# Performance work log

Hardware: AMD Instinct MI355X
Metric: run time of the kernel (lower is better)

Reference implementation:

```python
import jax, jax.numpy as jnp
import numpy as np

H = 128  # hidden size

def lstm_layer(x, Wih, Whh, bih, bhh):
    """One PyTorch-semantics LSTM layer. x: (B,T,F). Gate order: i,f,g,o."""
    B = x.shape[0]
    # Precompute input contributions for all timesteps: (B,T,4H)
    xg = jnp.einsum('btf,gf->btg', x, Wih) + bih + bhh
    def step(carry, xt):
        h, c = carry
        g = xt + h @ Whh.T                      # (B,4H)
        i, f, gg, o = jnp.split(g, 4, axis=-1)
        i = jax.nn.sigmoid(i)
        f = jax.nn.sigmoid(f)
        gg = jnp.tanh(gg)
        o = jax.nn.sigmoid(o)
        c = f * c + i * gg
        h = o * jnp.tanh(c)
        return (h, c), h
    h0 = jnp.zeros((B, H), x.dtype)
    (hT, cT), hs = jax.lax.scan(step, (h0, h0), jnp.swapaxes(xg, 0, 1))
    return jnp.swapaxes(hs, 0, 1), hT  # (B,T,H), (B,H)


def setup_inputs() -> dict:
    key = jax.random.key(0)
    ks = jax.random.split(key, 20)
    B, T = 256, 2048
    s = 1.0 / np.sqrt(H)  # PyTorch default init scale
    inp = {
        'x': jax.random.normal(ks[0], (B, T, 1), jnp.float32),
        'Wih0': jax.random.uniform(ks[1], (4 * H, 1), jnp.float32, -s, s),
        'Whh0': jax.random.uniform(ks[2], (4 * H, H), jnp.float32, -s, s),
        'bih0': jax.random.uniform(ks[3], (4 * H,), jnp.float32, -s, s),
        'bhh0': jax.random.uniform(ks[4], (4 * H,), jnp.float32, -s, s),
        'Wih1': jax.random.uniform(ks[5], (4 * H, H), jnp.float32, -s, s),
        'Whh1': jax.random.uniform(ks[6], (4 * H, H), jnp.float32, -s, s),
        'bih1': jax.random.uniform(ks[7], (4 * H,), jnp.float32, -s, s),
        'bhh1': jax.random.uniform(ks[8], (4 * H,), jnp.float32, -s, s),
        'Wih2': jax.random.uniform(ks[9], (4 * H, H), jnp.float32, -s, s),
        'Whh2': jax.random.uniform(ks[10], (4 * H, H), jnp.float32, -s, s),
        'bih2': jax.random.uniform(ks[11], (4 * H,), jnp.float32, -s, s),
        'bhh2': jax.random.uniform(ks[12], (4 * H,), jnp.float32, -s, s),
        'fc1_w': jax.random.uniform(ks[13], (64, H), jnp.float32, -s, s),
        'fc1_b': jax.random.uniform(ks[14], (64,), jnp.float32, -s, s),
        'fc2_w': jax.random.uniform(ks[15], (5, 64), jnp.float32, -1.0 / 8, 1.0 / 8),
        'fc2_b': jax.random.uniform(ks[16], (5,), jnp.float32, -1.0 / 8, 1.0 / 8),
    }
    return inp


def reference(x, Wih0, Whh0, bih0, bhh0, Wih1, Whh1, bih1, bhh1,
              Wih2, Whh2, bih2, bhh2, fc1_w, fc1_b, fc2_w, fc2_b):
    # 3-layer LSTM (eval mode: inter-layer dropout is identity)
    h1, _ = lstm_layer(x, Wih0, Whh0, bih0, bhh0)
    h2, _ = lstm_layer(h1, Wih1, Whh1, bih1, bhh1)
    _, hT = lstm_layer(h2, Wih2, Whh2, bih2, bhh2)  # hn[-1]: (B,H)
    z = jax.nn.relu(hT @ fc1_w.T + fc1_b)
    return z @ fc2_w.T + fc2_b  # (B, num_classes)
```

## Files before the change

### kernel.cpp

```cpp
#include <hip/hip_runtime.h>

#define HDIM 128
#define TDIM 2048
#define BDIM 256
#define CHUNK 16
#define NT 512
#define XGP 20

typedef _Float16 half8_t __attribute__((ext_vector_type(8)));
typedef float f32x4 __attribute__((ext_vector_type(4)));

__device__ __forceinline__ f32x4 mfma16(half8_t a, half8_t b, f32x4 c) {
    return __builtin_amdgcn_mfma_f32_16x16x32_f16(a, b, c, 0, 0, 0);
}

__device__ __forceinline__ void fast_barrier() {
    asm volatile("s_waitcnt lgkmcnt(0)\n\ts_barrier" ::: "memory");
}

__device__ __forceinline__ float sigm_f(float x) { return 1.0f / (1.0f + __expf(-x)); }
__device__ __forceinline__ float tanh_f(float x) { return 1.0f - 2.0f / (1.0f + __expf(2.0f * x)); }

__global__ __launch_bounds__(256)
void convert_w(const float* __restrict__ Whh0, const float* __restrict__ Wih1,
               const float* __restrict__ Whh1, const float* __restrict__ Wih2,
               const float* __restrict__ Whh2, _Float16* __restrict__ dst) {
    int i = blockIdx.x * 256 + threadIdx.x;
    int seg = i >> 16, off = i & 65535;
    const float* s = (seg == 0) ? Whh0 : (seg == 1) ? Wih1 : (seg == 2) ? Whh1
                   : (seg == 3) ? Wih2 : Whh2;
    dst[i] = (_Float16)s[off];
}

__global__ __launch_bounds__(NT, 2)
void lstm3_kernel(const float* __restrict__ x,   const float* __restrict__ Wih0,
                  const float* __restrict__ bih0, const float* __restrict__ bhh0,
                  const float* __restrict__ bih1, const float* __restrict__ bhh1,
                  const float* __restrict__ bih2, const float* __restrict__ bhh2,
                  const float* __restrict__ fc1w, const float* __restrict__ fc1b,
                  const float* __restrict__ fc2w, const float* __restrict__ fc2b,
                  float* __restrict__ out,
                  _Float16* __restrict__ gbuf, const _Float16* __restrict__ wbuf)
{
    __shared__ __align__(16) _Float16 hwin_s[CHUNK][HDIM];
    __shared__ __align__(16) _Float16 xin_s[2][CHUNK][HDIM];
    __shared__ __align__(16) float xg_s[2][512 * XGP];
    __shared__ __align__(16) float z_s[64];

    const int tid = threadIdx.x;
    const int ln = tid & 63;
    const int wv = tid >> 6;
    const int n16 = ln & 15;
    const int kb = (ln >> 4) * 8;
    const int un = wv * 16 + n16;
    const int b = blockIdx.x;

    {
        float bsum[4], w0[4];
        half8_t bhh[4][4];
#pragma unroll
        for (int tau = 0; tau < 4; ++tau) {
            const int g = tau * HDIM + un;
            bsum[tau] = bih0[g] + bhh0[g];
            w0[tau] = Wih0[g];
#pragma unroll
            for (int kk = 0; kk < 4; ++kk)
                bhh[tau][kk] = *(const half8_t*)(wbuf + (size_t)g * HDIM + kk * 32 + kb);
        }
        if (tid < HDIM) hwin_s[CHUNK - 1][tid] = (_Float16)0.f;
        float c = 0.f;
        float4 xp[4];
        {
            const float4* xq = (const float4*)(x + (size_t)b * TDIM);
#pragma unroll
            for (int i = 0; i < 4; ++i) xp[i] = xq[i];
        }

#pragma unroll 1
        for (int t0 = 0; t0 < TDIM; t0 += CHUNK) {
            float xv[CHUNK];
#pragma unroll
            for (int i = 0; i < 4; ++i) {
                xv[4 * i] = xp[i].x; xv[4 * i + 1] = xp[i].y;
                xv[4 * i + 2] = xp[i].z; xv[4 * i + 3] = xp[i].w;
            }
            int tn = (t0 + CHUNK < TDIM) ? (t0 + CHUNK) : t0;
            const float4* xq = (const float4*)(x + (size_t)b * TDIM + tn);
#pragma unroll
            for (int i = 0; i < 4; ++i) xp[i] = xq[i];

#pragma unroll
            for (int tt = 0; tt < CHUNK; ++tt) {
                fast_barrier();
                const int t = t0 + tt, row = (t + CHUNK - 1) & 15;
                half8_t A0 = *(const half8_t*)&hwin_s[row][kb];
                half8_t A1 = *(const half8_t*)&hwin_s[row][32 + kb];
                half8_t A2 = *(const half8_t*)&hwin_s[row][64 + kb];
                half8_t A3 = *(const half8_t*)&hwin_s[row][96 + kb];
                float g4[4];
#pragma unroll
                for (int tau = 0; tau < 4; ++tau) {
                    f32x4 Cz = {0.f, 0.f, 0.f, 0.f};
                    Cz = mfma16(A0, bhh[tau][0], Cz);
                    Cz = mfma16(A1, bhh[tau][1], Cz);
                    Cz = mfma16(A2, bhh[tau][2], Cz);
                    Cz = mfma16(A3, bhh[tau][3], Cz);
                    g4[tau] = Cz[0];
                }
                float ig = sigm_f(g4[0] + xv[tt] * w0[0] + bsum[0]);
                float fg = sigm_f(g4[1] + xv[tt] * w0[1] + bsum[1]);
                float gg = tanh_f(g4[2] + xv[tt] * w0[2] + bsum[2]);
                float og = sigm_f(g4[3] + xv[tt] * w0[3] + bsum[3]);
                c = fg * c + ig * gg;
                if (kb == 0) hwin_s[t & 15][un] = (_Float16)(og * tanh_f(c));
            }
            fast_barrier();
            int2 v = ((const int2*)&hwin_s[0][0])[tid];
            ((int2*)(gbuf + ((size_t)b * TDIM + t0) * HDIM))[tid] = v;
        }
    }

#pragma unroll 1
    for (int layer = 1; layer < 3; ++layer) {
        const _Float16* whh_p = wbuf + (size_t)((layer == 1) ? 2 : 4) * 65536;
        const _Float16* wih_p = wbuf + (size_t)((layer == 1) ? 1 : 3) * 65536;
        const float* bih = (layer == 1) ? bih1 : bih2;
        const float* bhh = (layer == 1) ? bhh1 : bhh2;

        float bsum[4];
        half8_t bhhf[4][4], bihf[4][4];
#pragma unroll
        for (int tau = 0; tau < 4; ++tau) {
            const int g = tau * HDIM + un;
            bsum[tau] = bih[g] + bhh[g];
#pragma unroll
            for (int kk = 0; kk < 4; ++kk)
                bhhf[tau][kk] = *(const half8_t*)(whh_p + (size_t)g * HDIM + kk * 32 + kb);
            const int gp = (wv * 4 + tau) * 16 + n16;
#pragma unroll
            for (int kk = 0; kk < 4; ++kk)
                bihf[tau][kk] = *(const half8_t*)(wih_p + (size_t)gp * HDIM + kk * 32 + kb);
        }

        __syncthreads();
        if (tid < HDIM) hwin_s[CHUNK - 1][tid] = (_Float16)0.f;
        float c = 0.f;

        int2 stage = ((const int2*)(gbuf + (size_t)b * TDIM * HDIM))[tid];
        ((int2*)&xin_s[0][0][0])[tid] = stage;
        __syncthreads();
        {
            half8_t A0 = *(const half8_t*)&xin_s[0][n16][kb];
            half8_t A1 = *(const half8_t*)&xin_s[0][n16][32 + kb];
            half8_t A2 = *(const half8_t*)&xin_s[0][n16][64 + kb];
            half8_t A3 = *(const half8_t*)&xin_s[0][n16][96 + kb];
#pragma unroll
            for (int tau = 0; tau < 4; ++tau) {
                f32x4 a = {0.f, 0.f, 0.f, 0.f};
                a = mfma16(A0, bihf[tau][0], a);
                a = mfma16(A1, bihf[tau][1], a);
                a = mfma16(A2, bihf[tau][2], a);
                a = mfma16(A3, bihf[tau][3], a);
                const int g = (wv * 4 + tau) * 16 + n16;
                *(f32x4*)&xg_s[0][g * XGP + (kb >> 1)] = a;
            }
        }
        stage = ((const int2*)(gbuf + ((size_t)b * TDIM + CHUNK) * HDIM))[tid];

        f32x4 pacc[4];
#pragma unroll 1
        for (int t0 = 0; t0 < TDIM; t0 += CHUNK) {
            const int ci = t0 >> 4, rbuf = ci & 1, cb = rbuf ^ 1;
            ((int2*)&xin_s[cb][0][0])[tid] = stage;
            int tn = (t0 + 2 * CHUNK < TDIM) ? (t0 + 2 * CHUNK) : t0;
            stage = ((const int2*)(gbuf + ((size_t)b * TDIM + tn) * HDIM))[tid];

            float2 xgv[4];
#pragma unroll
            for (int tt = 0; tt < CHUNK; ++tt) {
                fast_barrier();
                const int t = t0 + tt, row = (t + CHUNK - 1) & 15;
                half8_t A0 = *(const half8_t*)&hwin_s[row][kb];
                half8_t A1 = *(const half8_t*)&hwin_s[row][32 + kb];
                half8_t A2 = *(const half8_t*)&hwin_s[row][64 + kb];
                half8_t A3 = *(const half8_t*)&hwin_s[row][96 + kb];

                if (tt == 0) {
                    half8_t X0 = *(const half8_t*)&xin_s[cb][n16][kb];
                    half8_t X1 = *(const half8_t*)&xin_s[cb][n16][32 + kb];
                    half8_t X2 = *(const half8_t*)&xin_s[cb][n16][64 + kb];
                    half8_t X3 = *(const half8_t*)&xin_s[cb][n16][96 + kb];
#pragma unroll
                    for (int tau = 0; tau < 4; ++tau) {
                        f32x4 a = {0.f, 0.f, 0.f, 0.f};
                        a = mfma16(X0, bihf[tau][0], a);
                        a = mfma16(X1, bihf[tau][1], a);
                        a = mfma16(X2, bihf[tau][2], a);
                        a = mfma16(X3, bihf[tau][3], a);
                        pacc[tau] = a;
                    }
                }
                if ((tt & 1) == 0) {
#pragma unroll
                    for (int q = 0; q < 4; ++q)
                        xgv[q] = *(const float2*)&xg_s[rbuf][(q * HDIM + un) * XGP + tt];
                }

                float g4[4];
#pragma unroll
                for (int tau = 0; tau < 4; ++tau) {
                    f32x4 Cz = {0.f, 0.f, 0.f, 0.f};
                    Cz = mfma16(A0, bhhf[tau][0], Cz);
                    Cz = mfma16(A1, bhhf[tau][1], Cz);
                    Cz = mfma16(A2, bhhf[tau][2], Cz);
                    Cz = mfma16(A3, bhhf[tau][3], Cz);
                    g4[tau] = Cz[0];
                }

                float x0 = (tt & 1) ? xgv[0].y : xgv[0].x;
                float x1 = (tt & 1) ? xgv[1].y : xgv[1].x;
                float x2 = (tt & 1) ? xgv[2].y : xgv[2].x;
                float x3 = (tt & 1) ? xgv[3].y : xgv[3].x;
                float ig = sigm_f(g4[0] + x0 + bsum[0]);
                float fg = sigm_f(g4[1] + x1 + bsum[1]);
                float gg = tanh_f(g4[2] + x2 + bsum[2]);
                float og = sigm_f(g4[3] + x3 + bsum[3]);
                c = fg * c + ig * gg;
                if (kb == 0) hwin_s[t & 15][un] = (_Float16)(og * tanh_f(c));

                if (tt == CHUNK - 1) {
#pragma unroll
                    for (int tau = 0; tau < 4; ++tau) {
                        const int g = (wv * 4 + tau) * 16 + n16;
                        *(f32x4*)&xg_s[cb][g * XGP + (kb >> 1)] = pacc[tau];
                    }
                }
            }
            if (layer == 1) {
                fast_barrier();
                int2 v = ((const int2*)&hwin_s[0][0])[tid];
                ((int2*)(gbuf + ((size_t)b * TDIM + t0) * HDIM))[tid] = v;
            }
        }
    }

    __syncthreads();
    if (tid < 64) {
        const float* w = fc1w + tid * HDIM;
        float s = fc1b[tid];
#pragma unroll
        for (int k = 0; k < HDIM; ++k) s += w[k] * (float)hwin_s[CHUNK - 1][k];
        z_s[tid] = fmaxf(s, 0.0f);
    }
    __syncthreads();
    if (tid < 5) {
        const float* w = fc2w + tid * 64;
        float s = fc2b[tid];
#pragma unroll
        for (int k = 0; k < 64; ++k) s += w[k] * z_s[k];
        out[b * 5 + tid] = s;
    }
}

extern "C" void kernel_launch(void* const* d_in, const int* in_sizes, int n_in,
                              void* d_out, int out_size, void* d_ws, size_t ws_size,
                              hipStream_t stream) {
    (void)in_sizes; (void)n_in; (void)out_size; (void)ws_size;
    const float* x    = (const float*)d_in[0];
    const float* Wih0 = (const float*)d_in[1];
    const float* Whh0 = (const float*)d_in[2];
    const float* bih0 = (const float*)d_in[3];
    const float* bhh0 = (const float*)d_in[4];
    const float* Wih1 = (const float*)d_in[5];
    const float* Whh1 = (const float*)d_in[6];
    const float* bih1 = (const float*)d_in[7];
    const float* bhh1 = (const float*)d_in[8];
    const float* Wih2 = (const float*)d_in[9];
    const float* Whh2 = (const float*)d_in[10];
    const float* bih2 = (const float*)d_in[11];
    const float* bhh2 = (const float*)d_in[12];
    const float* fc1w = (const float*)d_in[13];
    const float* fc1b = (const float*)d_in[14];
    const float* fc2w = (const float*)d_in[15];
    const float* fc2b = (const float*)d_in[16];
    float* out = (float*)d_out;

    _Float16* gbuf = (_Float16*)d_ws;
    _Float16* wbuf = gbuf + (size_t)67108864;

    hipLaunchKernelGGL(convert_w, dim3(1280), dim3(256), 0, stream,
                       Whh0, Wih1, Whh1, Wih2, Whh2, wbuf);
    hipLaunchKernelGGL(lstm3_kernel, dim3(BDIM), dim3(NT), 0, stream,
                       x, Wih0, bih0, bhh0, bih1, bhh1, bih2, bhh2,
                       fc1w, fc1b, fc2w, fc2b, out, gbuf, wbuf);
}
```

Measured before the change: 3.658 ms.

## Halve block to 256 threads, two hidden units per lane, Whh pinned in AGPRs

The block shrinks from 8 to 4 waves, so each lane now handles two hidden units. The recurrent Whh fragments are pinned in accumulator registers and fed to MFMA through inline asm. The input-projection weights are no longer held in registers; they are reloaded from global memory once per chunk. The goal is to cut per-step barrier cost and wave count on the serial recurrence, and the three layers are merged into one loop. In exchange each wave does twice the MFMA and activation work per step, adds hand-inserted s_nop hazard padding, and adds extra global loads for Wih.

```diff
diff --git a/kernel.cpp b/kernel.cpp
--- a/kernel.cpp
+++ b/kernel.cpp
@@ -3,8 +3,8 @@
 #define HDIM 128
 #define TDIM 2048
 #define BDIM 256
+#define NT 256
 #define CHUNK 16
-#define NT 512
 #define XGP 20
 
 typedef _Float16 half8_t __attribute__((ext_vector_type(8)));
@@ -13,6 +13,10 @@
 __device__ __forceinline__ f32x4 mfma16(half8_t a, half8_t b, f32x4 c) {
     return __builtin_amdgcn_mfma_f32_16x16x32_f16(a, b, c, 0, 0, 0);
 }
+__device__ __forceinline__ void mfma_agpr(f32x4 &d, half8_t a, half8_t b) {
+    asm("v_mfma_f32_16x16x32_f16 %0, %1, %2, %0" : "+v"(d) : "v"(a), "a"(b));
+}
+__device__ __forceinline__ void pin_agpr(half8_t &v) { asm("" : "+a"(v)); }
 
 __device__ __forceinline__ void fast_barrier() {
     asm volatile("s_waitcnt lgkmcnt(0)\n\ts_barrier" ::: "memory");
@@ -32,7 +36,7 @@
     dst[i] = (_Float16)s[off];
 }
 
-__global__ __launch_bounds__(NT, 2)
+__global__ __launch_bounds__(NT, 1)
 void lstm3_kernel(const float* __restrict__ x,   const float* __restrict__ Wih0,
                   const float* __restrict__ bih0, const float* __restrict__ bhh0,
                   const float* __restrict__ bih1, const float* __restrict__ bhh1,
@@ -47,48 +51,96 @@
     __shared__ __align__(16) float xg_s[2][512 * XGP];
     __shared__ __align__(16) float z_s[64];
 
-    const int tid = threadIdx.x;
-    const int ln = tid & 63;
-    const int wv = tid >> 6;
-    const int n16 = ln & 15;
-    const int kb = (ln >> 4) * 8;
-    const int un = wv * 16 + n16;
+    const int tid = threadIdx.x, ln = tid & 63, wv = tid >> 6;
+    const int n16 = ln & 15, qd = ln >> 4, kb = qd * 8;
+    const int un0 = wv * 32 + n16, un1 = un0 + 16;
     const int b = blockIdx.x;
 
-    {
-        float bsum[4], w0[4];
-        half8_t bhh[4][4];
-#pragma unroll
-        for (int tau = 0; tau < 4; ++tau) {
-            const int g = tau * HDIM + un;
-            bsum[tau] = bih0[g] + bhh0[g];
-            w0[tau] = Wih0[g];
-#pragma unroll
-            for (int kk = 0; kk < 4; ++kk)
-                bhh[tau][kk] = *(const half8_t*)(wbuf + (size_t)g * HDIM + kk * 32 + kb);
+    const _Float16* whhL[3] = {wbuf, wbuf + 2 * 65536, wbuf + 4 * 65536};
+    const _Float16* wihL[3] = {nullptr, wbuf + 1 * 65536, wbuf + 3 * 65536};
+    const float* bihL[3] = {bih0, bih1, bih2};
+    const float* bhhL[3] = {bhh0, bhh1, bhh2};
+
+    half8_t whh[2][4][4];
+
+#pragma unroll 1
+    for (int layer = 0; layer < 3; ++layer) {
+        float bsum[2][4], w0[2][4];
+#pragma unroll
+        for (int ug = 0; ug < 2; ++ug) {
+            const int un = (ug == 0) ? un0 : un1;
+#pragma unroll
+            for (int q = 0; q < 4; ++q) {
+                const int row = q * HDIM + un;
+                bsum[ug][q] = bihL[layer][row] + bhhL[layer][row];
+                w0[ug][q] = (layer == 0) ? Wih0[row] : 0.f;
+#pragma unroll
+                for (int kk = 0; kk < 4; ++kk) {
+                    whh[ug][q][kk] =
+                        *(const half8_t*)(whhL[layer] + (size_t)row * HDIM + kk * 32 + kb);
+                    pin_agpr(whh[ug][q][kk]);
+                }
+            }
         }
+
+        __syncthreads();
         if (tid < HDIM) hwin_s[CHUNK - 1][tid] = (_Float16)0.f;
-        float c = 0.f;
+        float c0 = 0.f, c1 = 0.f;
+
         float4 xp[4];
-        {
+        int4 stage = {0, 0, 0, 0};
+        if (layer == 0) {
             const float4* xq = (const float4*)(x + (size_t)b * TDIM);
 #pragma unroll
             for (int i = 0; i < 4; ++i) xp[i] = xq[i];
+            __syncthreads();
+        } else {
+            stage = ((const int4*)(gbuf + (size_t)b * TDIM * HDIM))[tid];
+            ((int4*)&xin_s[0][0][0])[tid] = stage;
+            __syncthreads();
+            half8_t X0 = *(const half8_t*)&xin_s[0][n16][kb];
+            half8_t X1 = *(const half8_t*)&xin_s[0][n16][32 + kb];
+            half8_t X2 = *(const half8_t*)&xin_s[0][n16][64 + kb];
+            half8_t X3 = *(const half8_t*)&xin_s[0][n16][96 + kb];
+#pragma unroll 1
+            for (int j = 0; j < 8; ++j) {
+                const int gp = (8 * wv + j) * 16 + n16;
+                const _Float16* wr = wihL[layer] + (size_t)gp * HDIM + kb;
+                half8_t w0f = *(const half8_t*)(wr);
+                half8_t w1f = *(const half8_t*)(wr + 32);
+                half8_t w2f = *(const half8_t*)(wr + 64);
+                half8_t w3f = *(const half8_t*)(wr + 96);
+                f32x4 a = {0.f, 0.f, 0.f, 0.f};
+                a = mfma16(X0, w0f, a);
+                a = mfma16(X1, w1f, a);
+                a = mfma16(X2, w2f, a);
+                a = mfma16(X3, w3f, a);
+                *(f32x4*)&xg_s[0][gp * XGP + qd * 4] = a;
+            }
+            stage = ((const int4*)(gbuf + ((size_t)b * TDIM + CHUNK) * HDIM))[tid];
         }
 
 #pragma unroll 1
         for (int t0 = 0; t0 < TDIM; t0 += CHUNK) {
+            const int ci = t0 >> 4, rbuf = ci & 1, cb = rbuf ^ 1;
             float xv[CHUNK];
-#pragma unroll
-            for (int i = 0; i < 4; ++i) {
-                xv[4 * i] = xp[i].x; xv[4 * i + 1] = xp[i].y;
-                xv[4 * i + 2] = xp[i].z; xv[4 * i + 3] = xp[i].w;
-            }
-            int tn = (t0 + CHUNK < TDIM) ? (t0 + CHUNK) : t0;
-            const float4* xq = (const float4*)(x + (size_t)b * TDIM + tn);
-#pragma unroll
-            for (int i = 0; i < 4; ++i) xp[i] = xq[i];
-
+            if (layer == 0) {
+#pragma unroll
+                for (int i = 0; i < 4; ++i) {
+                    xv[4 * i] = xp[i].x; xv[4 * i + 1] = xp[i].y;
+                    xv[4 * i + 2] = xp[i].z; xv[4 * i + 3] = xp[i].w;
+                }
+                int tn = (t0 + CHUNK < TDIM) ? (t0 + CHUNK) : t0;
+                const float4* xq = (const float4*)(x + (size_t)b * TDIM + tn);
+#pragma unroll
+                for (int i = 0; i < 4; ++i) xp[i] = xq[i];
+            } else {
+                ((int4*)&xin_s[cb][0][0])[tid] = stage;
+                int tn = (t0 + 2 * CHUNK < TDIM) ? (t0 + 2 * CHUNK) : t0;
+                stage = ((const int4*)(gbuf + ((size_t)b * TDIM + tn) * HDIM))[tid];
+            }
+
+            float2 xgv[2][4];
 #pragma unroll
             for (int tt = 0; tt < CHUNK; ++tt) {
                 fast_barrier();
@@ -97,149 +149,78 @@
                 half8_t A1 = *(const half8_t*)&hwin_s[row][32 + kb];
                 half8_t A2 = *(const half8_t*)&hwin_s[row][64 + kb];
                 half8_t A3 = *(const half8_t*)&hwin_s[row][96 + kb];
-                float g4[4];
-#pragma unroll
-                for (int tau = 0; tau < 4; ++tau) {
-                    f32x4 Cz = {0.f, 0.f, 0.f, 0.f};
-                    Cz = mfma16(A0, bhh[tau][0], Cz);
-                    Cz = mfma16(A1, bhh[tau][1], Cz);
-                    Cz = mfma16(A2, bhh[tau][2], Cz);
-                    Cz = mfma16(A3, bhh[tau][3], Cz);
-                    g4[tau] = Cz[0];
-                }
-                float ig = sigm_f(g4[0] + xv[tt] * w0[0] + bsum[0]);
-                float fg = sigm_f(g4[1] + xv[tt] * w0[1] + bsum[1]);
-                float gg = tanh_f(g4[2] + xv[tt] * w0[2] + bsum[2]);
-                float og = sigm_f(g4[3] + xv[tt] * w0[3] + bsum[3]);
-                c = fg * c + ig * gg;
-                if (kb == 0) hwin_s[t & 15][un] = (_Float16)(og * tanh_f(c));
-            }
-            fast_barrier();
-            int2 v = ((const int2*)&hwin_s[0][0])[tid];
-            ((int2*)(gbuf + ((size_t)b * TDIM + t0) * HDIM))[tid] = v;
-        }
-    }
-
-#pragma unroll 1
-    for (int layer = 1; layer < 3; ++layer) {
-        const _Float16* whh_p = wbuf + (size_t)((layer == 1) ? 2 : 4) * 65536;
-        const _Float16* wih_p = wbuf + (size_t)((layer == 1) ? 1 : 3) * 65536;
-        const float* bih = (layer == 1) ? bih1 : bih2;
-        const float* bhh = (layer == 1) ? bhh1 : bhh2;
-
-        float bsum[4];
-        half8_t bhhf[4][4], bihf[4][4];
-#pragma unroll
-        for (int tau = 0; tau < 4; ++tau) {
-            const int g = tau * HDIM + un;
-            bsum[tau] = bih[g] + bhh[g];
-#pragma unroll
-            for (int kk = 0; kk < 4; ++kk)
-                bhhf[tau][kk] = *(const half8_t*)(whh_p + (size_t)g * HDIM + kk * 32 + kb);
-            const int gp = (wv * 4 + tau) * 16 + n16;
-#pragma unroll
-            for (int kk = 0; kk < 4; ++kk)
-                bihf[tau][kk] = *(const half8_t*)(wih_p + (size_t)gp * HDIM + kk * 32 + kb);
-        }
-
-        __syncthreads();
-        if (tid < HDIM) hwin_s[CHUNK - 1][tid] = (_Float16)0.f;
-        float c = 0.f;
-
-        int2 stage = ((const int2*)(gbuf + (size_t)b * TDIM * HDIM))[tid];
-        ((int2*)&xin_s[0][0][0])[tid] = stage;
-        __syncthreads();
-        {
-            half8_t A0 = *(const half8_t*)&xin_s[0][n16][kb];
-            half8_t A1 = *(const half8_t*)&xin_s[0][n16][32 + kb];
-            half8_t A2 = *(const half8_t*)&xin_s[0][n16][64 + kb];
-            half8_t A3 = *(const half8_t*)&xin_s[0][n16][96 + kb];
-#pragma unroll
-            for (int tau = 0; tau < 4; ++tau) {
-                f32x4 a = {0.f, 0.f, 0.f, 0.f};
-                a = mfma16(A0, bihf[tau][0], a);
-                a = mfma16(A1, bihf[tau][1], a);
-                a = mfma16(A2, bihf[tau][2], a);
-                a = mfma16(A3, bihf[tau][3], a);
-                const int g = (wv * 4 + tau) * 16 + n16;
-                *(f32x4*)&xg_s[0][g * XGP + (kb >> 1)] = a;
-            }
-        }
-        stage = ((const int2*)(gbuf + ((size_t)b * TDIM + CHUNK) * HDIM))[tid];
-
-        f32x4 pacc[4];
-#pragma unroll 1
-        for (int t0 = 0; t0 < TDIM; t0 += CHUNK) {
-            const int ci = t0 >> 4, rbuf = ci & 1, cb = rbuf ^ 1;
-            ((int2*)&xin_s[cb][0][0])[tid] = stage;
-            int tn = (t0 + 2 * CHUNK < TDIM) ? (t0 + 2 * CHUNK) : t0;
-            stage = ((const int2*)(gbuf + ((size_t)b * TDIM + tn) * HDIM))[tid];
-
-            float2 xgv[4];
-#pragma unroll
-            for (int tt = 0; tt < CHUNK; ++tt) {
-                fast_barrier();
-                const int t = t0 + tt, row = (t + CHUNK - 1) & 15;
-                half8_t A0 = *(const half8_t*)&hwin_s[row][kb];
-                half8_t A1 = *(const half8_t*)&hwin_s[row][32 + kb];
-                half8_t A2 = *(const half8_t*)&hwin_s[row][64 + kb];
-                half8_t A3 = *(const half8_t*)&hwin_s[row][96 + kb];
-
-                if (tt == 0) {
+
+                if (layer > 0 && tt == 0) {
                     half8_t X0 = *(const half8_t*)&xin_s[cb][n16][kb];
                     half8_t X1 = *(const half8_t*)&xin_s[cb][n16][32 + kb];
                     half8_t X2 = *(const half8_t*)&xin_s[cb][n16][64 + kb];
                     half8_t X3 = *(const half8_t*)&xin_s[cb][n16][96 + kb];
-#pragma unroll
-                    for (int tau = 0; tau < 4; ++tau) {
+#pragma unroll 1
+                    for (int j = 0; j < 8; ++j) {
+                        const int gp = (8 * wv + j) * 16 + n16;
+                        const _Float16* wr = wihL[layer] + (size_t)gp * HDIM + kb;
+                        half8_t w0f = *(const half8_t*)(wr);
+                        half8_t w1f = *(const half8_t*)(wr + 32);
+                        half8_t w2f = *(const half8_t*)(wr + 64);
+                        half8_t w3f = *(const half8_t*)(wr + 96);
                         f32x4 a = {0.f, 0.f, 0.f, 0.f};
-                        a = mfma16(X0, bihf[tau][0], a);
-                        a = mfma16(X1, bihf[tau][1], a);
-                        a = mfma16(X2, bihf[tau][2], a);
-                        a = mfma16(X3, bihf[tau][3], a);
-                        pacc[tau] = a;
+                        a = mfma16(X0, w0f, a);
+                        a = mfma16(X1, w1f, a);
+                        a = mfma16(X2, w2f, a);
+                        a = mfma16(X3, w3f, a);
+                        *(f32x4*)&xg_s[cb][gp * XGP + qd * 4] = a;
                     }
                 }
-                if ((tt & 1) == 0) {
-#pragma unroll
-                    for (int q = 0; q < 4; ++q)
-                        xgv[q] = *(const float2*)&xg_s[rbuf][(q * HDIM + un) * XGP + tt];
-                }
-
-                float g4[4];
-#pragma unroll
-                for (int tau = 0; tau < 4; ++tau) {
-                    f32x4 Cz = {0.f, 0.f, 0.f, 0.f};
-                    Cz = mfma16(A0, bhhf[tau][0], Cz);
-                    Cz = mfma16(A1, bhhf[tau][1], Cz);
-                    Cz = mfma16(A2, bhhf[tau][2], Cz);
-                    Cz = mfma16(A3, bhhf[tau][3], Cz);
-                    g4[tau] = Cz[0];
-                }
-
-                float x0 = (tt & 1) ? xgv[0].y : xgv[0].x;
-                float x1 = (tt & 1) ? xgv[1].y : xgv[1].x;
-                float x2 = (tt & 1) ? xgv[2].y : xgv[2].x;
-                float x3 = (tt & 1) ? xgv[3].y : xgv[3].x;
-                float ig = sigm_f(g4[0] + x0 + bsum[0]);
-                float fg = sigm_f(g4[1] + x1 + bsum[1]);
-                float gg = tanh_f(g4[2] + x2 + bsum[2]);
-                float og = sigm_f(g4[3] + x3 + bsum[3]);
-                c = fg * c + ig * gg;
-                if (kb == 0) hwin_s[t & 15][un] = (_Float16)(og * tanh_f(c));
-
-                if (tt == CHUNK - 1) {
-#pragma unroll
-                    for (int tau = 0; tau < 4; ++tau) {
-                        const int g = (wv * 4 + tau) * 16 + n16;
-                        *(f32x4*)&xg_s[cb][g * XGP + (kb >> 1)] = pacc[tau];
+                if (layer > 0 && (tt & 1) == 0) {
+#pragma unroll
+                    for (int ug = 0; ug < 2; ++ug)
+#pragma unroll
+                        for (int q = 0; q < 4; ++q)
+                            xgv[ug][q] = *(const float2*)
+                                &xg_s[rbuf][(q * HDIM + ((ug == 0) ? un0 : un1)) * XGP + tt];
+                }
+
+                f32x4 d[2][4];
+#pragma unroll
+                for (int ug = 0; ug < 2; ++ug)
+#pragma unroll
+                    for (int q = 0; q < 4; ++q) {
+                        d[ug][q] = (f32x4){0.f, 0.f, 0.f, 0.f};
+                        mfma_agpr(d[ug][q], A0, whh[ug][q][0]);
+                        mfma_agpr(d[ug][q], A1, whh[ug][q][1]);
+                        mfma_agpr(d[ug][q], A2, whh[ug][q][2]);
+                        mfma_agpr(d[ug][q], A3, whh[ug][q][3]);
                     }
-                }
-            }
-            if (layer == 1) {
+                asm volatile("s_nop 7\n\ts_nop 7"
+                             : "+v"(d[0][0]), "+v"(d[0][1]), "+v"(d[0][2]), "+v"(d[0][3]),
+                               "+v"(d[1][0]), "+v"(d[1][1]), "+v"(d[1][2]), "+v"(d[1][3]));
+
+#pragma unroll
+                for (int ug = 0; ug < 2; ++ug) {
+                    float xq[4];
+                    if (layer == 0) {
+#pragma unroll
+                        for (int q = 0; q < 4; ++q) xq[q] = xv[tt] * w0[ug][q];
+                    } else {
+#pragma unroll
+                        for (int q = 0; q < 4; ++q)
+                            xq[q] = (tt & 1) ? xgv[ug][q].y : xgv[ug][q].x;
+                    }
+                    float ig = sigm_f(d[ug][0][0] + xq[0] + bsum[ug][0]);
+                    float fg = sigm_f(d[ug][1][0] + xq[1] + bsum[ug][1]);
+                    float gg = tanh_f(d[ug][2][0] + xq[2] + bsum[ug][2]);
+                    float og = sigm_f(d[ug][3][0] + xq[3] + bsum[ug][3]);
+                    float& cc = (ug == 0) ? c0 : c1;
+                    cc = fg * cc + ig * gg;
+                    if (qd == 0)
+                        hwin_s[t & 15][(ug == 0) ? un0 : un1] = (_Float16)(og * tanh_f(cc));
+                }
+            }
+
+            if (layer < 2) {
                 fast_barrier();
-                int2 v = ((const int2*)&hwin_s[0][0])[tid];
-                ((int2*)(gbuf + ((size_t)b * TDIM + t0) * HDIM))[tid] = v;
+                int4 v = ((const int4*)&hwin_s[0][0])[tid];
+                ((int4*)(gbuf + ((size_t)b * TDIM + t0) * HDIM))[tid] = v;
             }
         }
     }
@@ -247,18 +228,18 @@
     __syncthreads();
     if (tid < 64) {
         const float* w = fc1w + tid * HDIM;
-        float s = fc1b[tid];
-#pragma unroll
-        for (int k = 0; k < HDIM; ++k) s += w[k] * (float)hwin_s[CHUNK - 1][k];
-        z_s[tid] = fmaxf(s, 0.0f);
+        float sacc = fc1b[tid];
+#pragma unroll
+        for (int k = 0; k < HDIM; ++k) sacc += w[k] * (float)hwin_s[CHUNK - 1][k];
+        z_s[tid] = fmaxf(sacc, 0.0f);
     }
     __syncthreads();
     if (tid < 5) {
         const float* w = fc2w + tid * 64;
-        float s = fc2b[tid];
-#pragma unroll
-        for (int k = 0; k < 64; ++k) s += w[k] * z_s[k];
-        out[b * 5 + tid] = s;
+        float sacc = fc2b[tid];
+#pragma unroll
+        for (int k = 0; k < 64; ++k) sacc += w[k] * z_s[k];
+        out[b * 5 + tid] = sacc;
     }
 }
 
```

New measurement: 6.152 ms. 1.68x slower.

## Pin recurrent weights in AGPRs and stream input weights from global per chunk

Applied to the files above, without the earlier changes.

Recurrent Whh fragments are pinned in AGPRs, and the hidden-state MFMAs use inline asm that reads B from AGPRs. A fixed s_nop delay replaces compiler-managed dependency tracking. The register-resident Wih fragments are dropped: the next chunk's input projection is now spread over the first four timesteps of each chunk, with weights loaded from global/L2. Precomputed gate inputs are read four timesteps at a time. The aim is to free VGPR pressure and shorten the serial per-step path, at the cost of extra global weight traffic and hand-timed hazard nops.

```diff
diff --git a/kernel.cpp b/kernel.cpp
--- a/kernel.cpp
+++ b/kernel.cpp
@@ -13,6 +13,10 @@
 __device__ __forceinline__ f32x4 mfma16(half8_t a, half8_t b, f32x4 c) {
     return __builtin_amdgcn_mfma_f32_16x16x32_f16(a, b, c, 0, 0, 0);
 }
+__device__ __forceinline__ void mfma_agpr(f32x4 &d, half8_t a, half8_t b) {
+    asm("v_mfma_f32_16x16x32_f16 %0, %1, %2, %0" : "+v"(d) : "v"(a), "a"(b));
+}
+__device__ __forceinline__ void pin_agpr(half8_t &v) { asm("" : "+a"(v)); }
 
 __device__ __forceinline__ void fast_barrier() {
     asm volatile("s_waitcnt lgkmcnt(0)\n\ts_barrier" ::: "memory");
@@ -51,7 +55,8 @@
     const int ln = tid & 63;
     const int wv = tid >> 6;
     const int n16 = ln & 15;
-    const int kb = (ln >> 4) * 8;
+    const int qd = ln >> 4;
+    const int kb = qd * 8;
     const int un = wv * 16 + n16;
     const int b = blockIdx.x;
 
@@ -64,8 +69,10 @@
             bsum[tau] = bih0[g] + bhh0[g];
             w0[tau] = Wih0[g];
 #pragma unroll
-            for (int kk = 0; kk < 4; ++kk)
+            for (int kk = 0; kk < 4; ++kk) {
                 bhh[tau][kk] = *(const half8_t*)(wbuf + (size_t)g * HDIM + kk * 32 + kb);
+                pin_agpr(bhh[tau][kk]);
+            }
         }
         if (tid < HDIM) hwin_s[CHUNK - 1][tid] = (_Float16)0.f;
         float c = 0.f;
@@ -97,22 +104,23 @@
                 half8_t A1 = *(const half8_t*)&hwin_s[row][32 + kb];
                 half8_t A2 = *(const half8_t*)&hwin_s[row][64 + kb];
                 half8_t A3 = *(const half8_t*)&hwin_s[row][96 + kb];
-                float g4[4];
-#pragma unroll
-                for (int tau = 0; tau < 4; ++tau) {
-                    f32x4 Cz = {0.f, 0.f, 0.f, 0.f};
-                    Cz = mfma16(A0, bhh[tau][0], Cz);
-                    Cz = mfma16(A1, bhh[tau][1], Cz);
-                    Cz = mfma16(A2, bhh[tau][2], Cz);
-                    Cz = mfma16(A3, bhh[tau][3], Cz);
-                    g4[tau] = Cz[0];
-                }
-                float ig = sigm_f(g4[0] + xv[tt] * w0[0] + bsum[0]);
-                float fg = sigm_f(g4[1] + xv[tt] * w0[1] + bsum[1]);
-                float gg = tanh_f(g4[2] + xv[tt] * w0[2] + bsum[2]);
-                float og = sigm_f(g4[3] + xv[tt] * w0[3] + bsum[3]);
+                f32x4 d0 = {0,0,0,0}, d1 = {0,0,0,0}, d2 = {0,0,0,0}, d3 = {0,0,0,0};
+                mfma_agpr(d0, A0, bhh[0][0]); mfma_agpr(d0, A1, bhh[0][1]);
+                mfma_agpr(d0, A2, bhh[0][2]); mfma_agpr(d0, A3, bhh[0][3]);
+                mfma_agpr(d1, A0, bhh[1][0]); mfma_agpr(d1, A1, bhh[1][1]);
+                mfma_agpr(d1, A2, bhh[1][2]); mfma_agpr(d1, A3, bhh[1][3]);
+                mfma_agpr(d2, A0, bhh[2][0]); mfma_agpr(d2, A1, bhh[2][1]);
+                mfma_agpr(d2, A2, bhh[2][2]); mfma_agpr(d2, A3, bhh[2][3]);
+                mfma_agpr(d3, A0, bhh[3][0]); mfma_agpr(d3, A1, bhh[3][1]);
+                mfma_agpr(d3, A2, bhh[3][2]); mfma_agpr(d3, A3, bhh[3][3]);
+                asm volatile("s_nop 7\n\ts_nop 7"
+                             : "+v"(d0), "+v"(d1), "+v"(d2), "+v"(d3));
+                float ig = sigm_f(d0[0] + xv[tt] * w0[0] + bsum[0]);
+                float fg = sigm_f(d1[0] + xv[tt] * w0[1] + bsum[1]);
+                float gg = tanh_f(d2[0] + xv[tt] * w0[2] + bsum[2]);
+                float og = sigm_f(d3[0] + xv[tt] * w0[3] + bsum[3]);
                 c = fg * c + ig * gg;
-                if (kb == 0) hwin_s[t & 15][un] = (_Float16)(og * tanh_f(c));
+                if (qd == 0) hwin_s[t & 15][un] = (_Float16)(og * tanh_f(c));
             }
             fast_barrier();
             int2 v = ((const int2*)&hwin_s[0][0])[tid];
@@ -128,18 +136,16 @@
         const float* bhh = (layer == 1) ? bhh1 : bhh2;
 
         float bsum[4];
-        half8_t bhhf[4][4], bihf[4][4];
+        half8_t bhhf[4][4];
 #pragma unroll
         for (int tau = 0; tau < 4; ++tau) {
             const int g = tau * HDIM + un;
             bsum[tau] = bih[g] + bhh[g];
 #pragma unroll
-            for (int kk = 0; kk < 4; ++kk)
+            for (int kk = 0; kk < 4; ++kk) {
                 bhhf[tau][kk] = *(const half8_t*)(whh_p + (size_t)g * HDIM + kk * 32 + kb);
-            const int gp = (wv * 4 + tau) * 16 + n16;
-#pragma unroll
-            for (int kk = 0; kk < 4; ++kk)
-                bihf[tau][kk] = *(const half8_t*)(wih_p + (size_t)gp * HDIM + kk * 32 + kb);
+                pin_agpr(bhhf[tau][kk]);
+            }
         }
 
         __syncthreads();
@@ -150,24 +156,24 @@
         ((int2*)&xin_s[0][0][0])[tid] = stage;
         __syncthreads();
         {
-            half8_t A0 = *(const half8_t*)&xin_s[0][n16][kb];
-            half8_t A1 = *(const half8_t*)&xin_s[0][n16][32 + kb];
-            half8_t A2 = *(const half8_t*)&xin_s[0][n16][64 + kb];
-            half8_t A3 = *(const half8_t*)&xin_s[0][n16][96 + kb];
-#pragma unroll
-            for (int tau = 0; tau < 4; ++tau) {
+            half8_t X0 = *(const half8_t*)&xin_s[0][n16][kb];
+            half8_t X1 = *(const half8_t*)&xin_s[0][n16][32 + kb];
+            half8_t X2 = *(const half8_t*)&xin_s[0][n16][64 + kb];
+            half8_t X3 = *(const half8_t*)&xin_s[0][n16][96 + kb];
+#pragma unroll
+            for (int q = 0; q < 4; ++q) {
+                const int g = q * HDIM + un;
+                const _Float16* wr = wih_p + (size_t)g * HDIM + kb;
                 f32x4 a = {0.f, 0.f, 0.f, 0.f};
-                a = mfma16(A0, bihf[tau][0], a);
-                a = mfma16(A1, bihf[tau][1], a);
-                a = mfma16(A2, bihf[tau][2], a);
-                a = mfma16(A3, bihf[tau][3], a);
-                const int g = (wv * 4 + tau) * 16 + n16;
-                *(f32x4*)&xg_s[0][g * XGP + (kb >> 1)] = a;
+                a = mfma16(X0, *(const half8_t*)(wr),      a);
+                a = mfma16(X1, *(const half8_t*)(wr + 32), a);
+                a = mfma16(X2, *(const half8_t*)(wr + 64), a);
+                a = mfma16(X3, *(const half8_t*)(wr + 96), a);
+                *(f32x4*)&xg_s[0][g * XGP + qd * 4] = a;
             }
         }
         stage = ((const int2*)(gbuf + ((size_t)b * TDIM + CHUNK) * HDIM))[tid];
 
-        f32x4 pacc[4];
 #pragma unroll 1
         for (int t0 = 0; t0 < TDIM; t0 += CHUNK) {
             const int ci = t0 >> 4, rbuf = ci & 1, cb = rbuf ^ 1;
@@ -175,7 +181,8 @@
             int tn = (t0 + 2 * CHUNK < TDIM) ? (t0 + 2 * CHUNK) : t0;
             stage = ((const int2*)(gbuf + ((size_t)b * TDIM + tn) * HDIM))[tid];
 
-            float2 xgv[4];
+            half8_t XF0, XF1, XF2, XF3;
+            f32x4 xgq[4];
 #pragma unroll
             for (int tt = 0; tt < CHUNK; ++tt) {
                 fast_barrier();
@@ -186,55 +193,46 @@
                 half8_t A3 = *(const half8_t*)&hwin_s[row][96 + kb];
 
                 if (tt == 0) {
-                    half8_t X0 = *(const half8_t*)&xin_s[cb][n16][kb];
-                    half8_t X1 = *(const half8_t*)&xin_s[cb][n16][32 + kb];
-                    half8_t X2 = *(const half8_t*)&xin_s[cb][n16][64 + kb];
-                    half8_t X3 = *(const half8_t*)&xin_s[cb][n16][96 + kb];
-#pragma unroll
-                    for (int tau = 0; tau < 4; ++tau) {
-                        f32x4 a = {0.f, 0.f, 0.f, 0.f};
-                        a = mfma16(X0, bihf[tau][0], a);
-                        a = mfma16(X1, bihf[tau][1], a);
-                        a = mfma16(X2, bihf[tau][2], a);
-                        a = mfma16(X3, bihf[tau][3], a);
-                        pacc[tau] = a;
-                    }
+                    XF0 = *(const half8_t*)&xin_s[cb][n16][kb];
+                    XF1 = *(const half8_t*)&xin_s[cb][n16][32 + kb];
+                    XF2 = *(const half8_t*)&xin_s[cb][n16][64 + kb];
+                    XF3 = *(const half8_t*)&xin_s[cb][n16][96 + kb];
                 }
-                if ((tt & 1) == 0) {
+                if (tt < 4) {
+                    const int g = tt * HDIM + un;
+                    const _Float16* wr = wih_p + (size_t)g * HDIM + kb;
+                    f32x4 a = {0.f, 0.f, 0.f, 0.f};
+                    a = mfma16(XF0, *(const half8_t*)(wr),      a);
+                    a = mfma16(XF1, *(const half8_t*)(wr + 32), a);
+                    a = mfma16(XF2, *(const half8_t*)(wr + 64), a);
+                    a = mfma16(XF3, *(const half8_t*)(wr + 96), a);
+                    *(f32x4*)&xg_s[cb][g * XGP + qd * 4] = a;
+                }
+                if ((tt & 3) == 0) {
 #pragma unroll
                     for (int q = 0; q < 4; ++q)
-                        xgv[q] = *(const float2*)&xg_s[rbuf][(q * HDIM + un) * XGP + tt];
+                        xgq[q] = *(const f32x4*)&xg_s[rbuf][(q * HDIM + un) * XGP + tt];
                 }
 
-                float g4[4];
-#pragma unroll
-                for (int tau = 0; tau < 4; ++tau) {
-                    f32x4 Cz = {0.f, 0.f, 0.f, 0.f};
-                    Cz = mfma16(A0, bhhf[tau][0], Cz);
-                    Cz = mfma16(A1, bhhf[tau][1], Cz);
-                    Cz = mfma16(A2, bhhf[tau][2], Cz);
-                    Cz = mfma16(A3, bhhf[tau][3], Cz);
-                    g4[tau] = Cz[0];
-                }
-
-                float x0 = (tt & 1) ? xgv[0].y : xgv[0].x;
-                float x1 = (tt & 1) ? xgv[1].y : xgv[1].x;
-                float x2 = (tt & 1) ? xgv[2].y : xgv[2].x;
-                float x3 = (tt & 1) ? xgv[3].y : xgv[3].x;
-                float ig = sigm_f(g4[0] + x0 + bsum[0]);
-                float fg = sigm_f(g4[1] + x1 + bsum[1]);
-                float gg = tanh_f(g4[2] + x2 + bsum[2]);
-                float og = sigm_f(g4[3] + x3 + bsum[3]);
+                f32x4 d0 = {0,0,0,0}, d1 = {0,0,0,0}, d2 = {0,0,0,0}, d3 = {0,0,0,0};
+                mfma_agpr(d0, A0, bhhf[0][0]); mfma_agpr(d0, A1, bhhf[0][1]);
+                mfma_agpr(d0, A2, bhhf[0][2]); mfma_agpr(d0, A3, bhhf[0][3]);
+                mfma_agpr(d1, A0, bhhf[1][0]); mfma_agpr(d1, A1, bhhf[1][1]);
+                mfma_agpr(d1, A2, bhhf[1][2]); mfma_agpr(d1, A3, bhhf[1][3]);
+                mfma_agpr(d2, A0, bhhf[2][0]); mfma_agpr(d2, A1, bhhf[2][1]);
+                mfma_agpr(d2, A2, bhhf[2][2]); mfma_agpr(d2, A3, bhhf[2][3]);
+                mfma_agpr(d3, A0, bhhf[3][0]); mfma_agpr(d3, A1, bhhf[3][1]);
+                mfma_agpr(d3, A2, bhhf[3][2]); mfma_agpr(d3, A3, bhhf[3][3]);
+                asm volatile("s_nop 7\n\ts_nop 7"
+                             : "+v"(d0), "+v"(d1), "+v"(d2), "+v"(d3));
+
+                const int sel = tt & 3;
+                float ig = sigm_f(d0[0] + xgq[0][sel] + bsum[0]);
+                float fg = sigm_f(d1[0] + xgq[1][sel] + bsum[1]);
+                float gg = tanh_f(d2[0] + xgq[2][sel] + bsum[2]);
+                float og = sigm_f(d3[0] + xgq[3][sel] + bsum[3]);
                 c = fg * c + ig * gg;
-                if (kb == 0) hwin_s[t & 15][un] = (_Float16)(og * tanh_f(c));
-
-                if (tt == CHUNK - 1) {
-#pragma unroll
-                    for (int tau = 0; tau < 4; ++tau) {
-                        const int g = (wv * 4 + tau) * 16 + n16;
-                        *(f32x4*)&xg_s[cb][g * XGP + (kb >> 1)] = pacc[tau];
-                    }
-                }
+                if (qd == 0) hwin_s[t & 15][un] = (_Float16)(og * tanh_f(c));
             }
             if (layer == 1) {
                 fast_barrier();
@@ -247,18 +245,18 @@
     __syncthreads();
     if (tid < 64) {
         const float* w = fc1w + tid * HDIM;
-        float s = fc1b[tid];
-#pragma unroll
-        for (int k = 0; k < HDIM; ++k) s += w[k] * (float)hwin_s[CHUNK - 1][k];
-        z_s[tid] = fmaxf(s, 0.0f);
+        float sacc = fc1b[tid];
+#pragma unroll
+        for (int k = 0; k < HDIM; ++k) sacc += w[k] * (float)hwin_s[CHUNK - 1][k];
+        z_s[tid] = fmaxf(sacc, 0.0f);
     }
     __syncthreads();
     if (tid < 5) {
         const float* w = fc2w + tid * 64;
-        float s = fc2b[tid];
-#pragma unroll
-        for (int k = 0; k < 64; ++k) s += w[k] * z_s[k];
-        out[b * 5 + tid] = s;
+        float sacc = fc2b[tid];
+#pragma unroll
+        for (int k = 0; k < 64; ++k) sacc += w[k] * z_s[k];
+        out[b * 5 + tid] = sacc;
     }
 }
 
```

Measured after the change: 3.901 ms. +6.7%, slower.
